# Kernel tuning notes

Hardware: AMD Instinct MI355X
Metric: run time of the kernel (lower is better)

Reference implementation:

```python
import jax, jax.numpy as jnp
import numpy as np

DK = 64

def setup_inputs() -> dict:
    key = jax.random.key(0)
    kq, kk, kv = jax.random.split(key, 3)
    B, S, dk, dv = 16, 2048, 64, 64
    q = jax.random.normal(kq, (B, S, dk), dtype=jnp.float32)
    k = jax.random.normal(kk, (B, S, dk), dtype=jnp.float32)
    v = jax.random.normal(kv, (B, S, dv), dtype=jnp.float32)
    return {"q": q, "k": k, "v": v}

def reference(q, k, v):
    # scores: [B, Sq, Sk], scaled by 1/sqrt(dk)
    scale = 1.0 / jnp.sqrt(jnp.asarray(DK, dtype=q.dtype))
    scores = jnp.einsum('bqd,bkd->bqk', q, k) * scale
    attn = jax.nn.softmax(scores, axis=-1)
    return jnp.einsum('bqk,bkd->bqd', attn, v)
```

## Files before the change

### kernel.cpp

```cpp
#include <hip/hip_runtime.h>
#include <hip/hip_fp16.h>

#define SLEN 2048

typedef _Float16 half8_t  __attribute__((ext_vector_type(8)));
typedef __fp16   fp16x2_t __attribute__((ext_vector_type(2)));
typedef float    floatx16 __attribute__((ext_vector_type(16)));
typedef float    float2v  __attribute__((ext_vector_type(2)));

#define MFMA(a, b, c) __builtin_amdgcn_mfma_f32_32x32x16_f16((a), (b), (c), 0, 0, 0)

typedef const __attribute__((address_space(1))) void gvoid_t;
typedef __attribute__((address_space(3))) void lvoid_t;

__device__ __forceinline__ void gload_lds16(const void* g, void* l) {
    __builtin_amdgcn_global_load_lds((gvoid_t*)g, (lvoid_t*)l, 16, 0, 0);
}

__device__ __forceinline__ int bswap23(int r) {
    return (r & ~12) | ((r & 4) << 1) | ((r & 8) >> 1);
}

#define QSCALE 0.18033688011112042f
#define CINIT  -5.770780163555854f

__device__ __forceinline__ floatx16 zero16() {
    floatx16 z;
    #pragma unroll
    for (int i = 0; i < 16; ++i) z[i] = 0.0f;
    return z;
}

__device__ __forceinline__ floatx16 initC() {
    floatx16 z;
    #pragma unroll
    for (int i = 0; i < 16; ++i) z[i] = CINIT;
    return z;
}

union PU { fp16x2_t h2[4]; half8_t h8; };

__global__ __launch_bounds__(256)
void prep_kernel(const float* __restrict__ Kg, const float* __restrict__ Vg,
                 _Float16* __restrict__ KP, _Float16* __restrict__ VP)
{
    __shared__ _Float16 kt[32][72];
    __shared__ _Float16 vt[32][72];
    const int t = threadIdx.x;
    const int T = blockIdx.x;
    const size_t row0 = (size_t)T * 32;

    {
        const int r = t >> 3, c0 = (t & 7) * 8;
        const float* kp = Kg + (row0 + r) * 64 + c0;
        const float* vp = Vg + (row0 + r) * 64 + c0;
        float4 a0 = *(const float4*)kp;
        float4 a1 = *(const float4*)(kp + 4);
        float4 b0 = *(const float4*)vp;
        float4 b1 = *(const float4*)(vp + 4);
        kt[r][c0 + 0] = (_Float16)a0.x; kt[r][c0 + 1] = (_Float16)a0.y;
        kt[r][c0 + 2] = (_Float16)a0.z; kt[r][c0 + 3] = (_Float16)a0.w;
        kt[r][c0 + 4] = (_Float16)a1.x; kt[r][c0 + 5] = (_Float16)a1.y;
        kt[r][c0 + 6] = (_Float16)a1.z; kt[r][c0 + 7] = (_Float16)a1.w;
        vt[r][c0 + 0] = (_Float16)b0.x; vt[r][c0 + 1] = (_Float16)b0.y;
        vt[r][c0 + 2] = (_Float16)b0.z; vt[r][c0 + 3] = (_Float16)b0.w;
        vt[r][c0 + 4] = (_Float16)b1.x; vt[r][c0 + 5] = (_Float16)b1.y;
        vt[r][c0 + 6] = (_Float16)b1.z; vt[r][c0 + 7] = (_Float16)b1.w;
    }
    __syncthreads();

    const int hi  = (t >> 5) & 1;
    const int col = t & 31;

    {
        const int dc = t >> 6;
        half8_t ko;
        #pragma unroll
        for (int j = 0; j < 8; ++j) ko[j] = kt[col][dc * 16 + hi * 8 + j];
        *(half8_t*)(KP + (size_t)T * 2048 + t * 8) = ko;
    }
    {
        const int g = t >> 6, kc = g & 1, nc = g >> 1;
        half8_t vo;
        #pragma unroll
        for (int j = 0; j < 8; ++j)
            vo[j] = vt[bswap23(kc * 16 + hi * 8 + j)][nc * 32 + col];
        *(half8_t*)(VP + (size_t)T * 2048 + t * 8) = vo;
    }
}

__global__ __launch_bounds__(256, 2)
void fattn_kernel(const float* __restrict__ Qg, const _Float16* __restrict__ KP,
                  const _Float16* __restrict__ VP, float* __restrict__ Og)
{
    __shared__ __align__(16) _Float16 ring[32768];
    __shared__ float lbufl[4][2][32];
    __shared__ float lbuf2[2][32];

    const int tid  = threadIdx.x;
    const int w    = tid >> 6;
    const int lane = tid & 63;
    const int h    = lane >> 5;
    const int col  = lane & 31;

    const int p  = blockIdx.x;
    const int b  = ((p >> 8) << 3) | (p & 7);
    const int qb = (p >> 3) & 31;

    half8_t qh[2][4];
    #pragma unroll
    for (int s = 0; s < 2; ++s) {
        const size_t qrow = (size_t)b * SLEN + (size_t)qb * 64 + s * 32 + col;
        const float* qp = Qg + qrow * 64 + h * 8;
        #pragma unroll
        for (int dc = 0; dc < 4; ++dc) {
            float4 f0 = *(const float4*)(qp + dc * 16);
            float4 f1 = *(const float4*)(qp + dc * 16 + 4);
            float v[8] = {f0.x, f0.y, f0.z, f0.w, f1.x, f1.y, f1.z, f1.w};
            #pragma unroll
            for (int j = 0; j < 8; ++j)
                qh[s][dc][j] = (_Float16)(v[j] * QSCALE);
        }
    }

    _Float16* myring = ring + w * 4096;
    const char* KPb = (const char*)KP;
    const char* VPb = (const char*)VP;

    auto stage = [&](int buf, int t) {
        const size_t off = ((size_t)(b * 64 + w * 16 + t)) << 12;
        const char* ks = KPb + off + lane * 16;
        _Float16* d = myring + buf * 2048;
        gload_lds16(ks,        d);
        gload_lds16(ks + 1024, d + 512);
        gload_lds16(ks + 2048, d + 1024);
        gload_lds16(ks + 3072, d + 1536);
    };

#define LOADV(T, VF) {                                                        \
    const size_t offv = ((size_t)(b * 64 + w * 16 + (T))) << 12;              \
    const _Float16* vs = (const _Float16*)(VPb + offv) + lane * 8;            \
    _Pragma("unroll")                                                         \
    for (int c = 0; c < 4; ++c) VF[c] = *(const half8_t*)(vs + c * 512); }

    floatx16 o00 = zero16(), o01 = zero16(), o10 = zero16(), o11 = zero16();
    float2v la0A = {0.0f, 0.0f}, la0B = {0.0f, 0.0f};
    float2v la1A = {0.0f, 0.0f}, la1B = {0.0f, 0.0f};

    half8_t vfA[4], vfB[4];

    stage(0, 0);
    LOADV(0, vfA)

#define EXPPK(SS, U, J, ACC) {                                        \
    float e0 = __builtin_amdgcn_exp2f(SS[2*(J)]);                     \
    float e1 = __builtin_amdgcn_exp2f(SS[2*(J)+1]);                   \
    float2v e2 = {e0, e1};                                            \
    ACC += e2;                                                        \
    (U).h2[(J) & 3] = __builtin_amdgcn_cvt_pkrtz(e0, e1); }

#define BODY(T, VFC, VFN)                                                     \
{                                                                             \
    const int cur = (T) & 1;                                                  \
    if ((T) < 15) {                                                           \
        stage(1 - cur, (T) + 1);                    \
        LOADV((T) + 1, VFN)                        \
        asm volatile("s_waitcnt vmcnt(8)" ::: "memory");    \
    } else {                                                                  \
        asm volatile("s_waitcnt vmcnt(0)" ::: "memory");                      \
    }                                                                         \
    _Float16* kb = myring + cur * 2048;                                       \
    half8_t kf[4];                                                            \
    _Pragma("unroll")                                                         \
    for (int dc = 0; dc < 4; ++dc)                                            \
        kf[dc] = *(half8_t*)(kb + dc * 512 + lane * 8);                       \
    floatx16 sa0 = zero16(), sb0 = initC();                                   \
    floatx16 sa1 = zero16(), sb1 = initC();                                   \
                                   \
    sa0 = MFMA(kf[0], qh[0][0], sa0);                                         \
    sb0 = MFMA(kf[2], qh[0][2], sb0);                                         \
    sa0 = MFMA(kf[1], qh[0][1], sa0);                                         \
    sb0 = MFMA(kf[3], qh[0][3], sb0);                                         \
                         \
    floatx16 ss0 = sa0 + sb0;                                                 \
    PU u0, u1;                                                                \
    sa1 = MFMA(kf[0], qh[1][0], sa1);                                         \
    EXPPK(ss0, u0, 0, la0A) EXPPK(ss0, u0, 1, la0B)                           \
    sb1 = MFMA(kf[2], qh[1][2], sb1);                                         \
    EXPPK(ss0, u0, 2, la0A) EXPPK(ss0, u0, 3, la0B)                           \
    sa1 = MFMA(kf[1], qh[1][1], sa1);                                         \
    EXPPK(ss0, u1, 4, la0A) EXPPK(ss0, u1, 5, la0B)                           \
    sb1 = MFMA(kf[3], qh[1][3], sb1);                                         \
    EXPPK(ss0, u1, 6, la0A) EXPPK(ss0, u1, 7, la0B)                           \
    half8_t pf00 = u0.h8, pf01 = u1.h8;                                       \
                         \
    floatx16 ss1 = sa1 + sb1;                                                 \
    PU u2, u3;                                                                \
    o00 = MFMA(pf00, VFC[0], o00);                                            \
    EXPPK(ss1, u2, 0, la1A) EXPPK(ss1, u2, 1, la1B)                           \
    o01 = MFMA(pf00, VFC[2], o01);                                            \
    EXPPK(ss1, u2, 2, la1A) EXPPK(ss1, u2, 3, la1B)                           \
    o00 = MFMA(pf01, VFC[1], o00);                                            \
    EXPPK(ss1, u3, 4, la1A) EXPPK(ss1, u3, 5, la1B)                           \
    o01 = MFMA(pf01, VFC[3], o01);                                            \
    EXPPK(ss1, u3, 6, la1A) EXPPK(ss1, u3, 7, la1B)                           \
    half8_t pf10 = u2.h8, pf11 = u3.h8;                                       \
                                                         \
    o10 = MFMA(pf10, VFC[0], o10);                                            \
    o11 = MFMA(pf10, VFC[2], o11);                                            \
    o10 = MFMA(pf11, VFC[1], o10);                                            \
    o11 = MFMA(pf11, VFC[3], o11);                                            \
}

    for (int t = 0; t < 16; t += 2) {
        BODY(t,     vfA, vfB);
        BODY(t + 1, vfB, vfA);
    }
#undef BODY
#undef EXPPK
#undef LOADV

    float la0 = la0A[0] + la0A[1] + la0B[0] + la0B[1];
    float la1 = la1A[0] + la1A[1] + la1B[0] + la1B[1];

    float lw0 = la0 + __shfl_xor(la0, 32, 64);
    float lw1 = la1 + __shfl_xor(la1, 32, 64);

    float* cb = (float*)ring;

#define ODUMP(d, g, acc) { _Pragma("unroll") \
    for (int r = 0; r < 16; ++r) (d)[(((g)*16 + r)*2 + h)*32 + col] = (acc)[r]; }
#define OADD(d, g, acc) { _Pragma("unroll") \
    for (int r = 0; r < 16; ++r) (acc)[r] += (d)[(((g)*16 + r)*2 + h)*32 + col]; }

    __syncthreads();
    if (w >= 2) {
        float* d = cb + (w - 2) * 4096;
        ODUMP(d, 0, o00) ODUMP(d, 1, o01) ODUMP(d, 2, o10) ODUMP(d, 3, o11)
        if (h == 0) { lbufl[w][0][col] = lw0; lbufl[w][1][col] = lw1; }
    }
    __syncthreads();
    if (w < 2) {
        float* d = cb + w * 4096;
        OADD(d, 0, o00) OADD(d, 1, o01) OADD(d, 2, o10) OADD(d, 3, o11)
        lw0 += lbufl[w + 2][0][col];
        lw1 += lbufl[w + 2][1][col];
    }
    __syncthreads();
    if (w == 1) {
        ODUMP(cb, 0, o00) ODUMP(cb, 1, o01) ODUMP(cb, 2, o10) ODUMP(cb, 3, o11)
        if (h == 0) { lbufl[1][0][col] = lw0; lbufl[1][1][col] = lw1; }
    }
    __syncthreads();
    if (w == 0) {
        OADD(cb, 0, o00) OADD(cb, 1, o01) OADD(cb, 2, o10) OADD(cb, 3, o11)
        lw0 += lbufl[1][0][col];
        lw1 += lbufl[1][1][col];
        if (h == 0) { lbuf2[0][col] = lw0; lbuf2[1][col] = lw1; }
    }
    __syncthreads();
    if (w == 0) {
        float* ob = cb + 8192;
        #pragma unroll
        for (int r = 0; r < 16; ++r) {
            const int qr = (r & 3) + 8 * (r >> 2) + 4 * h;
            const float li0 = 1.0f / lbuf2[0][qr];
            const float li1 = 1.0f / lbuf2[1][qr];
            ob[(0 * 32 + qr) * 64 +  0 + col] = o00[r] * li0;
            ob[(0 * 32 + qr) * 64 + 32 + col] = o01[r] * li0;
            ob[(1 * 32 + qr) * 64 +  0 + col] = o10[r] * li1;
            ob[(1 * 32 + qr) * 64 + 32 + col] = o11[r] * li1;
        }
    }
    __syncthreads();
    {
        const float* ob = cb + 8192;
        const int q = tid >> 2, ch = tid & 3;
        float4 x0 = *(const float4*)(ob + q * 64 + ch * 16);
        float4 x1 = *(const float4*)(ob + q * 64 + ch * 16 + 4);
        float4 x2 = *(const float4*)(ob + q * 64 + ch * 16 + 8);
        float4 x3 = *(const float4*)(ob + q * 64 + ch * 16 + 12);
        float* op = Og + ((size_t)b * SLEN + (size_t)qb * 64 + q) * 64 + ch * 16;
        *(float4*)(op)      = x0;
        *(float4*)(op + 4)  = x1;
        *(float4*)(op + 8)  = x2;
        *(float4*)(op + 12) = x3;
    }
#undef ODUMP
#undef OADD
}

extern "C" void kernel_launch(void* const* d_in, const int* in_sizes, int n_in,
                              void* d_out, int out_size, void* d_ws, size_t ws_size,
                              hipStream_t stream) {
    const float* q = (const float*)d_in[0];
    const float* k = (const float*)d_in[1];
    const float* v = (const float*)d_in[2];
    float* o = (float*)d_out;

    _Float16* KP = (_Float16*)d_ws;
    _Float16* VP = KP + (size_t)1024 * 2048;
    (void)ws_size; (void)in_sizes; (void)n_in; (void)out_size;

    prep_kernel<<<dim3(1024), dim3(256), 0, stream>>>(k, v, KP, VP);
    fattn_kernel<<<dim3(512), dim3(256), 0, stream>>>(q, KP, VP, o);
}
```

Measured before the change: 101.0 us.

## Prefetch next K tile into registers and chain score MFMAs off constant init

The attention loop now reads the next K tile from LDS into registers in the middle of the current iteration, after waiting on its async load. This takes the LDS read latency off the critical path at the start of each step. The score MFMAs now form one dependent chain seeded with the constant offset, replacing two parallel chains plus a vector add, which saves instructions but serialises the chain. The prep kernel handles two tiles per 512-thread block and uses vectorised 16-byte LDS writes and reads, at the cost of more register pressure from the extra K buffers.

New measurement: 104.9 us. +3.8%, slower.

```diff
diff --git a/kernel.cpp b/kernel.cpp
--- a/kernel.cpp
+++ b/kernel.cpp
@@ -23,6 +23,13 @@
 
 #define QSCALE 0.18033688011112042f
 #define CINIT  -5.770780163555854f
+
+__device__ __forceinline__ floatx16 initC() {
+    floatx16 z;
+    #pragma unroll
+    for (int i = 0; i < 16; ++i) z[i] = CINIT;
+    return z;
+}
 
 __device__ __forceinline__ floatx16 zero16() {
     floatx16 z;
@@ -31,23 +38,18 @@
     return z;
 }
 
-__device__ __forceinline__ floatx16 initC() {
-    floatx16 z;
-    #pragma unroll
-    for (int i = 0; i < 16; ++i) z[i] = CINIT;
-    return z;
-}
-
 union PU { fp16x2_t h2[4]; half8_t h8; };
 
-__global__ __launch_bounds__(256)
+__global__ __launch_bounds__(512)
 void prep_kernel(const float* __restrict__ Kg, const float* __restrict__ Vg,
                  _Float16* __restrict__ KP, _Float16* __restrict__ VP)
 {
-    __shared__ _Float16 kt[32][72];
-    __shared__ _Float16 vt[32][72];
-    const int t = threadIdx.x;
-    const int T = blockIdx.x;
+    __shared__ __align__(16) _Float16 kt[2][32][72];
+    __shared__ __align__(16) _Float16 vt[2][32][72];
+    const int tid = threadIdx.x;
+    const int sub = tid >> 8;
+    const int t   = tid & 255;
+    const int T   = blockIdx.x * 2 + sub;
     const size_t row0 = (size_t)T * 32;
 
     {
@@ -58,14 +60,17 @@
         float4 a1 = *(const float4*)(kp + 4);
         float4 b0 = *(const float4*)vp;
         float4 b1 = *(const float4*)(vp + 4);
-        kt[r][c0 + 0] = (_Float16)a0.x; kt[r][c0 + 1] = (_Float16)a0.y;
-        kt[r][c0 + 2] = (_Float16)a0.z; kt[r][c0 + 3] = (_Float16)a0.w;
-        kt[r][c0 + 4] = (_Float16)a1.x; kt[r][c0 + 5] = (_Float16)a1.y;
-        kt[r][c0 + 6] = (_Float16)a1.z; kt[r][c0 + 7] = (_Float16)a1.w;
-        vt[r][c0 + 0] = (_Float16)b0.x; vt[r][c0 + 1] = (_Float16)b0.y;
-        vt[r][c0 + 2] = (_Float16)b0.z; vt[r][c0 + 3] = (_Float16)b0.w;
-        vt[r][c0 + 4] = (_Float16)b1.x; vt[r][c0 + 5] = (_Float16)b1.y;
-        vt[r][c0 + 6] = (_Float16)b1.z; vt[r][c0 + 7] = (_Float16)b1.w;
+        half8_t k8, v8;
+        k8[0] = (_Float16)a0.x; k8[1] = (_Float16)a0.y;
+        k8[2] = (_Float16)a0.z; k8[3] = (_Float16)a0.w;
+        k8[4] = (_Float16)a1.x; k8[5] = (_Float16)a1.y;
+        k8[6] = (_Float16)a1.z; k8[7] = (_Float16)a1.w;
+        v8[0] = (_Float16)b0.x; v8[1] = (_Float16)b0.y;
+        v8[2] = (_Float16)b0.z; v8[3] = (_Float16)b0.w;
+        v8[4] = (_Float16)b1.x; v8[5] = (_Float16)b1.y;
+        v8[6] = (_Float16)b1.z; v8[7] = (_Float16)b1.w;
+        *(half8_t*)&kt[sub][r][c0] = k8;
+        *(half8_t*)&vt[sub][r][c0] = v8;
     }
     __syncthreads();
 
@@ -74,9 +79,7 @@
 
     {
         const int dc = t >> 6;
-        half8_t ko;
-        #pragma unroll
-        for (int j = 0; j < 8; ++j) ko[j] = kt[col][dc * 16 + hi * 8 + j];
+        half8_t ko = *(half8_t*)&kt[sub][col][dc * 16 + hi * 8];
         *(half8_t*)(KP + (size_t)T * 2048 + t * 8) = ko;
     }
     {
@@ -84,7 +87,7 @@
         half8_t vo;
         #pragma unroll
         for (int j = 0; j < 8; ++j)
-            vo[j] = vt[bswap23(kc * 16 + hi * 8 + j)][nc * 32 + col];
+            vo[j] = vt[sub][bswap23(kc * 16 + hi * 8 + j)][nc * 32 + col];
         *(half8_t*)(VP + (size_t)T * 2048 + t * 8) = vo;
     }
 }
@@ -143,14 +146,24 @@
     _Pragma("unroll")                                                         \
     for (int c = 0; c < 4; ++c) VF[c] = *(const half8_t*)(vs + c * 512); }
 
+#define LOADK(BUF, KF) {                                                      \
+    _Float16* kb_ = myring + (BUF) * 2048;                                    \
+    _Pragma("unroll")                                                         \
+    for (int dc = 0; dc < 4; ++dc)                                            \
+        KF[dc] = *(half8_t*)(kb_ + dc * 512 + lane * 8); }
+
     floatx16 o00 = zero16(), o01 = zero16(), o10 = zero16(), o11 = zero16();
     float2v la0A = {0.0f, 0.0f}, la0B = {0.0f, 0.0f};
     float2v la1A = {0.0f, 0.0f}, la1B = {0.0f, 0.0f};
 
-    half8_t vfA[4], vfB[4];
+    const floatx16 cv = initC();
+
+    half8_t kfA[4], kfB[4], vfA[4], vfB[4];
 
     stage(0, 0);
     LOADV(0, vfA)
+    asm volatile("s_waitcnt vmcnt(4)" ::: "memory");
+    LOADK(0, kfA)
 
 #define EXPPK(SS, U, J, ACC) {                                        \
     float e0 = __builtin_amdgcn_exp2f(SS[2*(J)]);                     \
@@ -159,52 +172,45 @@
     ACC += e2;                                                        \
     (U).h2[(J) & 3] = __builtin_amdgcn_cvt_pkrtz(e0, e1); }
 
-#define BODY(T, VFC, VFN)                                                     \
+#define BODY(T, KFC, KFN, VFC, VFN)                                           \
 {                                                                             \
     const int cur = (T) & 1;                                                  \
     if ((T) < 15) {                                                           \
         stage(1 - cur, (T) + 1);                    \
         LOADV((T) + 1, VFN)                        \
-        asm volatile("s_waitcnt vmcnt(8)" ::: "memory");    \
-    } else {                                                                  \
-        asm volatile("s_waitcnt vmcnt(0)" ::: "memory");                      \
     }                                                                         \
-    _Float16* kb = myring + cur * 2048;                                       \
-    half8_t kf[4];                                                            \
-    _Pragma("unroll")                                                         \
-    for (int dc = 0; dc < 4; ++dc)                                            \
-        kf[dc] = *(half8_t*)(kb + dc * 512 + lane * 8);                       \
-    floatx16 sa0 = zero16(), sb0 = initC();                                   \
-    floatx16 sa1 = zero16(), sb1 = initC();                                   \
-                                   \
-    sa0 = MFMA(kf[0], qh[0][0], sa0);                                         \
-    sb0 = MFMA(kf[2], qh[0][2], sb0);                                         \
-    sa0 = MFMA(kf[1], qh[0][1], sa0);                                         \
-    sb0 = MFMA(kf[3], qh[0][3], sb0);                                         \
-                         \
-    floatx16 ss0 = sa0 + sb0;                                                 \
+                \
+    floatx16 s0 = MFMA(KFC[0], qh[0][0], cv);                                 \
+    s0 = MFMA(KFC[1], qh[0][1], s0);                                          \
+    s0 = MFMA(KFC[2], qh[0][2], s0);                                          \
+    s0 = MFMA(KFC[3], qh[0][3], s0);                                          \
+                          \
     PU u0, u1;                                                                \
-    sa1 = MFMA(kf[0], qh[1][0], sa1);                                         \
-    EXPPK(ss0, u0, 0, la0A) EXPPK(ss0, u0, 1, la0B)                           \
-    sb1 = MFMA(kf[2], qh[1][2], sb1);                                         \
-    EXPPK(ss0, u0, 2, la0A) EXPPK(ss0, u0, 3, la0B)                           \
-    sa1 = MFMA(kf[1], qh[1][1], sa1);                                         \
-    EXPPK(ss0, u1, 4, la0A) EXPPK(ss0, u1, 5, la0B)                           \
-    sb1 = MFMA(kf[3], qh[1][3], sb1);                                         \
-    EXPPK(ss0, u1, 6, la0A) EXPPK(ss0, u1, 7, la0B)                           \
+    floatx16 s1 = MFMA(KFC[0], qh[1][0], cv);                                 \
+    EXPPK(s0, u0, 0, la0A) EXPPK(s0, u0, 1, la0B)                             \
+    s1 = MFMA(KFC[1], qh[1][1], s1);                                          \
+    EXPPK(s0, u0, 2, la0A) EXPPK(s0, u0, 3, la0B)                             \
+    s1 = MFMA(KFC[2], qh[1][2], s1);                                          \
+    EXPPK(s0, u1, 4, la0A) EXPPK(s0, u1, 5, la0B)                             \
+    s1 = MFMA(KFC[3], qh[1][3], s1);                                          \
+    EXPPK(s0, u1, 6, la0A) EXPPK(s0, u1, 7, la0B)                             \
     half8_t pf00 = u0.h8, pf01 = u1.h8;                                       \
-                         \
-    floatx16 ss1 = sa1 + sb1;                                                 \
+                                \
     PU u2, u3;                                                                \
     o00 = MFMA(pf00, VFC[0], o00);                                            \
-    EXPPK(ss1, u2, 0, la1A) EXPPK(ss1, u2, 1, la1B)                           \
+    EXPPK(s1, u2, 0, la1A) EXPPK(s1, u2, 1, la1B)                             \
     o01 = MFMA(pf00, VFC[2], o01);                                            \
-    EXPPK(ss1, u2, 2, la1A) EXPPK(ss1, u2, 3, la1B)                           \
+    EXPPK(s1, u2, 2, la1A) EXPPK(s1, u2, 3, la1B)                             \
     o00 = MFMA(pf01, VFC[1], o00);                                            \
-    EXPPK(ss1, u3, 4, la1A) EXPPK(ss1, u3, 5, la1B)                           \
+    EXPPK(s1, u3, 4, la1A) EXPPK(s1, u3, 5, la1B)                             \
     o01 = MFMA(pf01, VFC[3], o01);                                            \
-    EXPPK(ss1, u3, 6, la1A) EXPPK(ss1, u3, 7, la1B)                           \
+    EXPPK(s1, u3, 6, la1A) EXPPK(s1, u3, 7, la1B)                             \
     half8_t pf10 = u2.h8, pf11 = u3.h8;                                       \
+         \
+    if ((T) < 15) {                                                           \
+        asm volatile("s_waitcnt vmcnt(4)" ::: "memory");                      \
+        LOADK(1 - cur, KFN)                                                   \
+    }                                                                         \
                                                          \
     o10 = MFMA(pf10, VFC[0], o10);                                            \
     o11 = MFMA(pf10, VFC[2], o11);                                            \
@@ -213,11 +219,12 @@
 }
 
     for (int t = 0; t < 16; t += 2) {
-        BODY(t,     vfA, vfB);
-        BODY(t + 1, vfB, vfA);
+        BODY(t,     kfA, kfB, vfA, vfB);
+        BODY(t + 1, kfB, kfA, vfB, vfA);
     }
 #undef BODY
 #undef EXPPK
+#undef LOADK
 #undef LOADV
 
     float la0 = la0A[0] + la0A[1] + la0B[0] + la0B[1];
@@ -302,6 +309,6 @@
     _Float16* VP = KP + (size_t)1024 * 2048;
     (void)ws_size; (void)in_sizes; (void)n_in; (void)out_size;
 
-    prep_kernel<<<dim3(1024), dim3(256), 0, stream>>>(k, v, KP, VP);
+    prep_kernel<<<dim3(512), dim3(512), 0, stream>>>(k, v, KP, VP);
     fattn_kernel<<<dim3(512), dim3(256), 0, stream>>>(q, KP, VP, o);
 }
```

## Defer second PV MFMA group into next iteration; vectorize and widen prep kernel

Applied to the files above, without the earlier changes.

The last four PV MFMAs of each tile are carried into the next iteration, where they run before the next tile's loads and K-fragment reads, with a final drain after the loop. This lets the matrix core work overlap the wait on the next tile's data instead of sitting at the end of the exp chain. The prep kernel now handles two tiles per 512-thread block and uses 16-byte vector LDS writes and K reads in place of scalar element accesses. The deferred MFMAs keep two extra half8 fragments live across iterations, which adds register pressure at two waves per SIMD.

Measured after the change: 101.9 us. Within noise of the previous version (+0.9%).

```diff
diff --git a/kernel.cpp b/kernel.cpp
--- a/kernel.cpp
+++ b/kernel.cpp
@@ -40,14 +40,16 @@
 
 union PU { fp16x2_t h2[4]; half8_t h8; };
 
-__global__ __launch_bounds__(256)
+__global__ __launch_bounds__(512)
 void prep_kernel(const float* __restrict__ Kg, const float* __restrict__ Vg,
                  _Float16* __restrict__ KP, _Float16* __restrict__ VP)
 {
-    __shared__ _Float16 kt[32][72];
-    __shared__ _Float16 vt[32][72];
-    const int t = threadIdx.x;
-    const int T = blockIdx.x;
+    __shared__ __align__(16) _Float16 kt[2][32][72];
+    __shared__ __align__(16) _Float16 vt[2][32][72];
+    const int tid = threadIdx.x;
+    const int sub = tid >> 8;
+    const int t   = tid & 255;
+    const int T   = blockIdx.x * 2 + sub;
     const size_t row0 = (size_t)T * 32;
 
     {
@@ -58,14 +60,17 @@
         float4 a1 = *(const float4*)(kp + 4);
         float4 b0 = *(const float4*)vp;
         float4 b1 = *(const float4*)(vp + 4);
-        kt[r][c0 + 0] = (_Float16)a0.x; kt[r][c0 + 1] = (_Float16)a0.y;
-        kt[r][c0 + 2] = (_Float16)a0.z; kt[r][c0 + 3] = (_Float16)a0.w;
-        kt[r][c0 + 4] = (_Float16)a1.x; kt[r][c0 + 5] = (_Float16)a1.y;
-        kt[r][c0 + 6] = (_Float16)a1.z; kt[r][c0 + 7] = (_Float16)a1.w;
-        vt[r][c0 + 0] = (_Float16)b0.x; vt[r][c0 + 1] = (_Float16)b0.y;
-        vt[r][c0 + 2] = (_Float16)b0.z; vt[r][c0 + 3] = (_Float16)b0.w;
-        vt[r][c0 + 4] = (_Float16)b1.x; vt[r][c0 + 5] = (_Float16)b1.y;
-        vt[r][c0 + 6] = (_Float16)b1.z; vt[r][c0 + 7] = (_Float16)b1.w;
+        half8_t k8, v8;
+        k8[0] = (_Float16)a0.x; k8[1] = (_Float16)a0.y;
+        k8[2] = (_Float16)a0.z; k8[3] = (_Float16)a0.w;
+        k8[4] = (_Float16)a1.x; k8[5] = (_Float16)a1.y;
+        k8[6] = (_Float16)a1.z; k8[7] = (_Float16)a1.w;
+        v8[0] = (_Float16)b0.x; v8[1] = (_Float16)b0.y;
+        v8[2] = (_Float16)b0.z; v8[3] = (_Float16)b0.w;
+        v8[4] = (_Float16)b1.x; v8[5] = (_Float16)b1.y;
+        v8[6] = (_Float16)b1.z; v8[7] = (_Float16)b1.w;
+        *(half8_t*)&kt[sub][r][c0] = k8;
+        *(half8_t*)&vt[sub][r][c0] = v8;
     }
     __syncthreads();
 
@@ -74,9 +79,7 @@
 
     {
         const int dc = t >> 6;
-        half8_t ko;
-        #pragma unroll
-        for (int j = 0; j < 8; ++j) ko[j] = kt[col][dc * 16 + hi * 8 + j];
+        half8_t ko = *(half8_t*)&kt[sub][col][dc * 16 + hi * 8];
         *(half8_t*)(KP + (size_t)T * 2048 + t * 8) = ko;
     }
     {
@@ -84,7 +87,7 @@
         half8_t vo;
         #pragma unroll
         for (int j = 0; j < 8; ++j)
-            vo[j] = vt[bswap23(kc * 16 + hi * 8 + j)][nc * 32 + col];
+            vo[j] = vt[sub][bswap23(kc * 16 + hi * 8 + j)][nc * 32 + col];
         *(half8_t*)(VP + (size_t)T * 2048 + t * 8) = vo;
     }
 }
@@ -148,6 +151,7 @@
     float2v la1A = {0.0f, 0.0f}, la1B = {0.0f, 0.0f};
 
     half8_t vfA[4], vfB[4];
+    half8_t pf10c, pf11c;
 
     stage(0, 0);
     LOADV(0, vfA)
@@ -162,6 +166,13 @@
 #define BODY(T, VFC, VFN)                                                     \
 {                                                                             \
     const int cur = (T) & 1;                                                  \
+                    \
+    if ((T) > 0) {                                                            \
+        o10 = MFMA(pf10c, VFN[0], o10);                                       \
+        o11 = MFMA(pf10c, VFN[2], o11);                                       \
+        o10 = MFMA(pf11c, VFN[1], o10);                                       \
+        o11 = MFMA(pf11c, VFN[3], o11);                                       \
+    }                                                                         \
     if ((T) < 15) {                                                           \
         stage(1 - cur, (T) + 1);                    \
         LOADV((T) + 1, VFN)                        \
@@ -176,7 +187,7 @@
         kf[dc] = *(half8_t*)(kb + dc * 512 + lane * 8);                       \
     floatx16 sa0 = zero16(), sb0 = initC();                                   \
     floatx16 sa1 = zero16(), sb1 = initC();                                   \
-                                   \
+                     \
     sa0 = MFMA(kf[0], qh[0][0], sa0);                                         \
     sb0 = MFMA(kf[2], qh[0][2], sb0);                                         \
     sa0 = MFMA(kf[1], qh[0][1], sa0);                                         \
@@ -204,18 +215,19 @@
     EXPPK(ss1, u3, 4, la1A) EXPPK(ss1, u3, 5, la1B)                           \
     o01 = MFMA(pf01, VFC[3], o01);                                            \
     EXPPK(ss1, u3, 6, la1A) EXPPK(ss1, u3, 7, la1B)                           \
-    half8_t pf10 = u2.h8, pf11 = u3.h8;                                       \
-                                                         \
-    o10 = MFMA(pf10, VFC[0], o10);                                            \
-    o11 = MFMA(pf10, VFC[2], o11);                                            \
-    o10 = MFMA(pf11, VFC[1], o10);                                            \
-    o11 = MFMA(pf11, VFC[3], o11);                                            \
+        \
+    pf10c = u2.h8;                                                            \
+    pf11c = u3.h8;                                                            \
 }
 
     for (int t = 0; t < 16; t += 2) {
         BODY(t,     vfA, vfB);
         BODY(t + 1, vfB, vfA);
     }
+    o10 = MFMA(pf10c, vfB[0], o10);
+    o11 = MFMA(pf10c, vfB[2], o11);
+    o10 = MFMA(pf11c, vfB[1], o10);
+    o11 = MFMA(pf11c, vfB[3], o11);
 #undef BODY
 #undef EXPPK
 #undef LOADV
@@ -302,6 +314,6 @@
     _Float16* VP = KP + (size_t)1024 * 2048;
     (void)ws_size; (void)in_sizes; (void)n_in; (void)out_size;
 
-    prep_kernel<<<dim3(1024), dim3(256), 0, stream>>>(k, v, KP, VP);
+    prep_kernel<<<dim3(512), dim3(512), 0, stream>>>(k, v, KP, VP);
     fattn_kernel<<<dim3(512), dim3(256), 0, stream>>>(q, KP, VP, o);
 }
```
